# Performance work log

Hardware: AMD Instinct MI355X
Metric: run time of the kernel (lower is better)

The kernel has to match this reference:

```python
import jax, jax.numpy as jnp
import numpy as np

MARGIN_POS = 0.1
MARGIN_NEG = 0.8
HARD_RATIO = 0.3


def setup_inputs() -> dict:
    key = jax.random.key(0)
    k1, k2, k3 = jax.random.split(key, 3)
    B, D = 16384, 1024
    return {
        "q_neg_proj": jax.random.normal(k1, (B, D), dtype=jnp.float32),
        "d_pos": jax.random.normal(k2, (B, D), dtype=jnp.float32),
        "d_neg": jax.random.normal(k3, (B, D), dtype=jnp.float32),
    }


def reference(q_neg_proj, d_pos, d_neg):
    B = q_neg_proj.shape[0]
    num_hard = max(1, int(B * HARD_RATIO))

    # diag(q @ d.T) == rowwise dot product; avoid the BxB matmul
    diag_sim_pos = jnp.einsum("bd,bd->b", q_neg_proj, d_pos)
    diag_sim_neg = jnp.einsum("bd,bd->b", q_neg_proj, d_neg)

    # hardest positives: largest similarities
    hard_sim_pos, _ = jax.lax.top_k(diag_sim_pos, num_hard)
    loss_pos = jnp.mean(jax.nn.relu(hard_sim_pos - MARGIN_POS))

    # hardest negatives: smallest similarities (topk largest=False)
    neg_smallest, _ = jax.lax.top_k(-diag_sim_neg, num_hard)
    hard_sim_neg = -neg_smallest
    loss_neg = jnp.mean(jax.nn.relu(MARGIN_NEG - hard_sim_neg))

    total_loss = loss_pos + loss_neg
    return (total_loss, loss_pos, loss_neg)
```

## Files before the change

kernel.cpp:

```cpp
#include <hip/hip_runtime.h>

constexpr int B_ROWS = 16384;
constexpr int K_HARD = 4915;
constexpr float MARGIN_POS = 0.1f;
constexpr float MARGIN_NEG = 0.8f;

__global__ __launch_bounds__(256, 8) void dot_kernel(
    const float4* __restrict__ q,
    const float4* __restrict__ dp,
    const float4* __restrict__ dn,
    float* __restrict__ out_pos,
    float* __restrict__ out_neg)
{
    const int wave = (blockIdx.x * blockDim.x + threadIdx.x) >> 6;
    const int lane = threadIdx.x & 63;
    const int base = wave * 256 + lane;

    float4 qv[4], pv[4], nv[4];
#pragma unroll
    for (int it = 0; it < 4; ++it) qv[it] = q[base + it * 64];
#pragma unroll
    for (int it = 0; it < 4; ++it) pv[it] = dp[base + it * 64];
#pragma unroll
    for (int it = 0; it < 4; ++it) nv[it] = dn[base + it * 64];

    float sp = 0.f, sn = 0.f;
#pragma unroll
    for (int it = 0; it < 4; ++it) {
        sp += qv[it].x * pv[it].x + qv[it].y * pv[it].y
            + qv[it].z * pv[it].z + qv[it].w * pv[it].w;
        sn += qv[it].x * nv[it].x + qv[it].y * nv[it].y
            + qv[it].z * nv[it].z + qv[it].w * nv[it].w;
    }
#pragma unroll
    for (int off = 32; off; off >>= 1) {
        sp += __shfl_xor(sp, off);
        sn += __shfl_xor(sn, off);
    }
    if (lane == 0) {
        out_pos[wave] = sp;
        out_neg[wave] = sn;
    }
}

__device__ __forceinline__ unsigned f2key(float f) {
    unsigned u = __float_as_uint(f);
    return (u & 0x80000000u) ? ~u : (u | 0x80000000u);
}
__device__ __forceinline__ float key2f(unsigned k) {
    return __uint_as_float((k & 0x80000000u) ? (k & 0x7FFFFFFFu) : ~k);
}

__global__ __launch_bounds__(1024) void select_finalize_kernel(
    const float* __restrict__ ws_vals,
    float* __restrict__ out)
{
    __shared__ unsigned hist[256];
    __shared__ unsigned ebase[256];
    __shared__ unsigned s_prefix, s_m;
    __shared__ float    s_redf[16];
    __shared__ int      s_redc[16];
    __shared__ float    s_loss[2];

    const int tid  = threadIdx.x;
    const int lane = tid & 63;
    const int wid  = tid >> 6;

    for (int side = 0; side < 2; ++side) {
        const float4* v4 = (const float4*)(ws_vals + side * B_ROWS);

        unsigned key[16];
#pragma unroll
        for (int j = 0; j < 4; ++j) {
            float4 x = v4[tid + j * 1024];
            key[4 * j + 0] = f2key(x.x);
            key[4 * j + 1] = f2key(x.y);
            key[4 * j + 2] = f2key(x.z);
            key[4 * j + 3] = f2key(x.w);
        }

        unsigned m = side ? (unsigned)(K_HARD - 1) : (unsigned)(B_ROWS - K_HARD);
        unsigned prefix = 0;

        for (int r = 0; r < 4; ++r) {
            const unsigned shift = 24 - 8 * r;
            const unsigned pmask = (r == 0) ? 0u : (0xFFFFFFFFu << (32 - 8 * r));
            if (tid < 256) hist[tid] = 0;
            __syncthreads();
#pragma unroll
            for (int j = 0; j < 16; ++j)
                if ((key[j] & pmask) == prefix)
                    atomicAdd(&hist[(key[j] >> shift) & 255u], 1u);
            __syncthreads();

            if (wid == 0) {
                unsigned h0 = hist[4 * lane + 0];
                unsigned h1 = hist[4 * lane + 1];
                unsigned h2 = hist[4 * lane + 2];
                unsigned h3 = hist[4 * lane + 3];
                unsigned gsum = h0 + h1 + h2 + h3;
                unsigned inc = gsum;
#pragma unroll
                for (int off = 1; off < 64; off <<= 1) {
                    unsigned t = __shfl_up(inc, off);
                    if (lane >= off) inc += t;
                }
                unsigned ex = inc - gsum;
                ebase[4 * lane + 0] = ex;
                ebase[4 * lane + 1] = ex + h0;
                ebase[4 * lane + 2] = ex + h0 + h1;
                ebase[4 * lane + 3] = ex + h0 + h1 + h2;
            }
            __syncthreads();

            if (tid < 256) {
                unsigned lo = ebase[tid];
                unsigned hi = lo + hist[tid];
                if (lo <= m && m < hi) {
                    s_prefix = prefix | ((unsigned)tid << shift);
                    s_m = m - lo;
                }
            }
            __syncthreads();
            prefix = s_prefix;
            m = s_m;
        }

        const unsigned tkey = prefix;
        const float    tval = key2f(tkey);

        float lsum = 0.f;
        int cnt = 0;
#pragma unroll
        for (int j = 0; j < 16; ++j) {
            const bool sel = side ? (key[j] < tkey) : (key[j] > tkey);
            if (sel) {
                const float v = key2f(key[j]);
                lsum += side ? fmaxf(MARGIN_NEG - v, 0.f)
                             : fmaxf(v - MARGIN_POS, 0.f);
                cnt++;
            }
        }
#pragma unroll
        for (int off = 32; off; off >>= 1) {
            lsum += __shfl_xor(lsum, off);
            cnt  += __shfl_xor(cnt, off);
        }
        if (lane == 0) { s_redf[wid] = lsum; s_redc[wid] = cnt; }
        __syncthreads();
        if (tid == 0) {
            float tot = 0.f;
            int c = 0;
            for (int w = 0; w < 16; ++w) { tot += s_redf[w]; c += s_redc[w]; }
            const float ft = side ? fmaxf(MARGIN_NEG - tval, 0.f)
                                  : fmaxf(tval - MARGIN_POS, 0.f);
            s_loss[side] = (tot + (float)(K_HARD - c) * ft) / (float)K_HARD;
        }
        __syncthreads();
    }

    if (tid == 0) {
        const float lp = s_loss[0];
        const float ln = s_loss[1];
        out[0] = lp + ln;
        out[1] = lp;
        out[2] = ln;
    }
}

extern "C" void kernel_launch(void* const* d_in, const int* in_sizes, int n_in,
                              void* d_out, int out_size, void* d_ws, size_t ws_size,
                              hipStream_t stream) {
    const float4* q  = (const float4*)d_in[0];
    const float4* dp = (const float4*)d_in[1];
    const float4* dn = (const float4*)d_in[2];
    float* out = (float*)d_out;

    float* ws     = (float*)d_ws;
    float* ws_pos = ws;
    float* ws_neg = ws + B_ROWS;

    dot_kernel<<<(B_ROWS * 64) / 256, 256, 0, stream>>>(q, dp, dn, ws_pos, ws_neg);
    select_finalize_kernel<<<1, 1024, 0, stream>>>(ws_pos, out);
}
```

Before: 55.51 us.

## Issue dot loads via inline asm and run both radix selects together

The dot-product kernel now issues all twelve 16-byte global loads back-to-back in inline assembly with immediate offsets and a single wait, so every load is in flight at once. The selection kernel now runs the positive and negative radix-select passes interleaved in one loop over shared histograms, which halves the number of barrier-separated rounds in the single-block finalize. The inline asm bypasses compiler scheduling and assumes 32-bit offsets fit the buffers.

```diff
diff --git a/kernel.cpp b/kernel.cpp
--- a/kernel.cpp
+++ b/kernel.cpp
@@ -5,32 +5,52 @@
 constexpr float MARGIN_POS = 0.1f;
 constexpr float MARGIN_NEG = 0.8f;
 
+typedef float f32x4 __attribute__((ext_vector_type(4)));
+
 __global__ __launch_bounds__(256, 8) void dot_kernel(
-    const float4* __restrict__ q,
-    const float4* __restrict__ dp,
-    const float4* __restrict__ dn,
+    const float* __restrict__ q,
+    const float* __restrict__ dp,
+    const float* __restrict__ dn,
     float* __restrict__ out_pos,
     float* __restrict__ out_neg)
 {
     const int wave = (blockIdx.x * blockDim.x + threadIdx.x) >> 6;
     const int lane = threadIdx.x & 63;
-    const int base = wave * 256 + lane;
-
-    float4 qv[4], pv[4], nv[4];
-#pragma unroll
-    for (int it = 0; it < 4; ++it) qv[it] = q[base + it * 64];
-#pragma unroll
-    for (int it = 0; it < 4; ++it) pv[it] = dp[base + it * 64];
-#pragma unroll
-    for (int it = 0; it < 4; ++it) nv[it] = dn[base + it * 64];
+    const unsigned voff = (unsigned)wave * 4096u + (unsigned)lane * 16u;
+
+    f32x4 q0, q1, q2, q3, p0, p1, p2, p3, n0, n1, n2, n3;
+    asm volatile(
+        "global_load_dwordx4 %[Q0], %[VO], %[QB] offset:0\n\t"
+        "global_load_dwordx4 %[Q1], %[VO], %[QB] offset:1024\n\t"
+        "global_load_dwordx4 %[Q2], %[VO], %[QB] offset:2048\n\t"
+        "global_load_dwordx4 %[Q3], %[VO], %[QB] offset:3072\n\t"
+        "global_load_dwordx4 %[P0], %[VO], %[PB] offset:0\n\t"
+        "global_load_dwordx4 %[P1], %[VO], %[PB] offset:1024\n\t"
+        "global_load_dwordx4 %[P2], %[VO], %[PB] offset:2048\n\t"
+        "global_load_dwordx4 %[P3], %[VO], %[PB] offset:3072\n\t"
+        "global_load_dwordx4 %[N0], %[VO], %[NB] offset:0\n\t"
+        "global_load_dwordx4 %[N1], %[VO], %[NB] offset:1024\n\t"
+        "global_load_dwordx4 %[N2], %[VO], %[NB] offset:2048\n\t"
+        "global_load_dwordx4 %[N3], %[VO], %[NB] offset:3072\n\t"
+        "s_waitcnt vmcnt(0)"
+        : [Q0]"=&v"(q0), [Q1]"=&v"(q1), [Q2]"=&v"(q2), [Q3]"=&v"(q3),
+          [P0]"=&v"(p0), [P1]"=&v"(p1), [P2]"=&v"(p2), [P3]"=&v"(p3),
+          [N0]"=&v"(n0), [N1]"=&v"(n1), [N2]"=&v"(n2), [N3]"=&v"(n3)
+        : [VO]"v"(voff), [QB]"s"(q), [PB]"s"(dp), [NB]"s"(dn)
+    );
+
+    f32x4 qa[4] = {q0, q1, q2, q3};
+    f32x4 pa[4] = {p0, p1, p2, p3};
+    f32x4 na[4] = {n0, n1, n2, n3};
 
     float sp = 0.f, sn = 0.f;
 #pragma unroll
     for (int it = 0; it < 4; ++it) {
-        sp += qv[it].x * pv[it].x + qv[it].y * pv[it].y
-            + qv[it].z * pv[it].z + qv[it].w * pv[it].w;
-        sn += qv[it].x * nv[it].x + qv[it].y * nv[it].y
-            + qv[it].z * nv[it].z + qv[it].w * nv[it].w;
+#pragma unroll
+        for (int c = 0; c < 4; ++c) {
+            sp += qa[it][c] * pa[it][c];
+            sn += qa[it][c] * na[it][c];
+        }
     }
 #pragma unroll
     for (int off = 32; off; off >>= 1) {
@@ -55,125 +75,123 @@
     const float* __restrict__ ws_vals,
     float* __restrict__ out)
 {
-    __shared__ unsigned hist[256];
-    __shared__ unsigned ebase[256];
-    __shared__ unsigned s_prefix, s_m;
-    __shared__ float    s_redf[16];
-    __shared__ int      s_redc[16];
-    __shared__ float    s_loss[2];
+    __shared__ unsigned hist[2][256];
+    __shared__ unsigned ebase[2][256];
+    __shared__ unsigned s_prefix[2], s_m[2];
+    __shared__ float    s_rf[2][16];
+    __shared__ unsigned s_rc[2][16];
 
     const int tid  = threadIdx.x;
     const int lane = tid & 63;
     const int wid  = tid >> 6;
 
-    for (int side = 0; side < 2; ++side) {
-        const float4* v4 = (const float4*)(ws_vals + side * B_ROWS);
-
-        unsigned key[16];
-#pragma unroll
-        for (int j = 0; j < 4; ++j) {
-            float4 x = v4[tid + j * 1024];
-            key[4 * j + 0] = f2key(x.x);
-            key[4 * j + 1] = f2key(x.y);
-            key[4 * j + 2] = f2key(x.z);
-            key[4 * j + 3] = f2key(x.w);
-        }
-
-        unsigned m = side ? (unsigned)(K_HARD - 1) : (unsigned)(B_ROWS - K_HARD);
-        unsigned prefix = 0;
-
-        for (int r = 0; r < 4; ++r) {
-            const unsigned shift = 24 - 8 * r;
-            const unsigned pmask = (r == 0) ? 0u : (0xFFFFFFFFu << (32 - 8 * r));
-            if (tid < 256) hist[tid] = 0;
-            __syncthreads();
-#pragma unroll
-            for (int j = 0; j < 16; ++j)
-                if ((key[j] & pmask) == prefix)
-                    atomicAdd(&hist[(key[j] >> shift) & 255u], 1u);
-            __syncthreads();
-
-            if (wid == 0) {
-                unsigned h0 = hist[4 * lane + 0];
-                unsigned h1 = hist[4 * lane + 1];
-                unsigned h2 = hist[4 * lane + 2];
-                unsigned h3 = hist[4 * lane + 3];
-                unsigned gsum = h0 + h1 + h2 + h3;
-                unsigned inc = gsum;
-#pragma unroll
-                for (int off = 1; off < 64; off <<= 1) {
-                    unsigned t = __shfl_up(inc, off);
-                    if (lane >= off) inc += t;
-                }
-                unsigned ex = inc - gsum;
-                ebase[4 * lane + 0] = ex;
-                ebase[4 * lane + 1] = ex + h0;
-                ebase[4 * lane + 2] = ex + h0 + h1;
-                ebase[4 * lane + 3] = ex + h0 + h1 + h2;
+    const float4* vp = (const float4*)ws_vals;
+    const float4* vn = (const float4*)(ws_vals + B_ROWS);
+
+    unsigned kp[16], kn[16];
+#pragma unroll
+    for (int j = 0; j < 4; ++j) {
+        const float4 a = vp[tid + j * 1024];
+        const float4 b = vn[tid + j * 1024];
+        kp[4*j+0] = f2key(a.x); kp[4*j+1] = f2key(a.y);
+        kp[4*j+2] = f2key(a.z); kp[4*j+3] = f2key(a.w);
+        kn[4*j+0] = f2key(b.x); kn[4*j+1] = f2key(b.y);
+        kn[4*j+2] = f2key(b.z); kn[4*j+3] = f2key(b.w);
+    }
+
+    unsigned m0 = (unsigned)(B_ROWS - K_HARD), pre0 = 0;
+    unsigned m1 = (unsigned)(K_HARD - 1),      pre1 = 0;
+
+    for (int r = 0; r < 4; ++r) {
+        const unsigned shift = 24 - 8 * r;
+        const unsigned pmask = (r == 0) ? 0u : (0xFFFFFFFFu << (32 - 8 * r));
+        if (tid < 256) { hist[0][tid] = 0; hist[1][tid] = 0; }
+        __syncthreads();
+#pragma unroll
+        for (int j = 0; j < 16; ++j) {
+            if ((kp[j] & pmask) == pre0) atomicAdd(&hist[0][(kp[j] >> shift) & 255u], 1u);
+            if ((kn[j] & pmask) == pre1) atomicAdd(&hist[1][(kn[j] >> shift) & 255u], 1u);
+        }
+        __syncthreads();
+
+        if (wid < 2) {
+            const int s = wid;
+            const unsigned h0 = hist[s][4*lane+0], h1 = hist[s][4*lane+1];
+            const unsigned h2 = hist[s][4*lane+2], h3 = hist[s][4*lane+3];
+            const unsigned g = h0 + h1 + h2 + h3;
+            unsigned inc = g;
+#pragma unroll
+            for (int off = 1; off < 64; off <<= 1) {
+                const unsigned t = __shfl_up(inc, off);
+                if (lane >= off) inc += t;
             }
-            __syncthreads();
-
-            if (tid < 256) {
-                unsigned lo = ebase[tid];
-                unsigned hi = lo + hist[tid];
-                if (lo <= m && m < hi) {
-                    s_prefix = prefix | ((unsigned)tid << shift);
-                    s_m = m - lo;
-                }
+            const unsigned ex = inc - g;
+            ebase[s][4*lane+0] = ex;
+            ebase[s][4*lane+1] = ex + h0;
+            ebase[s][4*lane+2] = ex + h0 + h1;
+            ebase[s][4*lane+3] = ex + h0 + h1 + h2;
+        }
+        __syncthreads();
+
+        if (tid < 512) {
+            const int s = tid >> 8;
+            const int b = tid & 255;
+            const unsigned mm = s ? m1 : m0;
+            const unsigned lo = ebase[s][b];
+            const unsigned hi = lo + hist[s][b];
+            if (lo <= mm && mm < hi) {
+                s_prefix[s] = (s ? pre1 : pre0) | ((unsigned)b << shift);
+                s_m[s] = mm - lo;
             }
-            __syncthreads();
-            prefix = s_prefix;
-            m = s_m;
-        }
-
-        const unsigned tkey = prefix;
-        const float    tval = key2f(tkey);
-
-        float lsum = 0.f;
-        int cnt = 0;
-#pragma unroll
-        for (int j = 0; j < 16; ++j) {
-            const bool sel = side ? (key[j] < tkey) : (key[j] > tkey);
-            if (sel) {
-                const float v = key2f(key[j]);
-                lsum += side ? fmaxf(MARGIN_NEG - v, 0.f)
-                             : fmaxf(v - MARGIN_POS, 0.f);
-                cnt++;
-            }
-        }
-#pragma unroll
-        for (int off = 32; off; off >>= 1) {
-            lsum += __shfl_xor(lsum, off);
-            cnt  += __shfl_xor(cnt, off);
-        }
-        if (lane == 0) { s_redf[wid] = lsum; s_redc[wid] = cnt; }
-        __syncthreads();
-        if (tid == 0) {
-            float tot = 0.f;
-            int c = 0;
-            for (int w = 0; w < 16; ++w) { tot += s_redf[w]; c += s_redc[w]; }
-            const float ft = side ? fmaxf(MARGIN_NEG - tval, 0.f)
-                                  : fmaxf(tval - MARGIN_POS, 0.f);
-            s_loss[side] = (tot + (float)(K_HARD - c) * ft) / (float)K_HARD;
-        }
-        __syncthreads();
-    }
-
+        }
+        __syncthreads();
+        pre0 = s_prefix[0]; m0 = s_m[0];
+        pre1 = s_prefix[1]; m1 = s_m[1];
+    }
+
+    const unsigned tk0 = pre0, tk1 = pre1;
+    const float    tv0 = key2f(tk0), tv1 = key2f(tk1);
+
+    float lp = 0.f, ln = 0.f;
+    unsigned cp = 0, cn = 0;
+#pragma unroll
+    for (int j = 0; j < 16; ++j) {
+        if (kp[j] > tk0) { lp += fmaxf(key2f(kp[j]) - MARGIN_POS, 0.f); cp++; }
+        if (kn[j] < tk1) { ln += fmaxf(MARGIN_NEG - key2f(kn[j]), 0.f); cn++; }
+    }
+#pragma unroll
+    for (int off = 32; off; off >>= 1) {
+        lp += __shfl_xor(lp, off);  ln += __shfl_xor(ln, off);
+        cp += __shfl_xor(cp, off);  cn += __shfl_xor(cn, off);
+    }
+    if (lane == 0) {
+        s_rf[0][wid] = lp; s_rf[1][wid] = ln;
+        s_rc[0][wid] = cp; s_rc[1][wid] = cn;
+    }
+    __syncthreads();
     if (tid == 0) {
-        const float lp = s_loss[0];
-        const float ln = s_loss[1];
-        out[0] = lp + ln;
-        out[1] = lp;
-        out[2] = ln;
+        float tp = 0.f, tn = 0.f;
+        unsigned ccp = 0, ccn = 0;
+        for (int w = 0; w < 16; ++w) {
+            tp += s_rf[0][w]; tn += s_rf[1][w];
+            ccp += s_rc[0][w]; ccn += s_rc[1][w];
+        }
+        const float fp = fmaxf(tv0 - MARGIN_POS, 0.f);
+        const float fn = fmaxf(MARGIN_NEG - tv1, 0.f);
+        const float LP = (tp + (float)(K_HARD - (int)ccp) * fp) / (float)K_HARD;
+        const float LN = (tn + (float)(K_HARD - (int)ccn) * fn) / (float)K_HARD;
+        out[0] = LP + LN;
+        out[1] = LP;
+        out[2] = LN;
     }
 }
 
 extern "C" void kernel_launch(void* const* d_in, const int* in_sizes, int n_in,
                               void* d_out, int out_size, void* d_ws, size_t ws_size,
                               hipStream_t stream) {
-    const float4* q  = (const float4*)d_in[0];
-    const float4* dp = (const float4*)d_in[1];
-    const float4* dn = (const float4*)d_in[2];
+    const float* q  = (const float*)d_in[0];
+    const float* dp = (const float*)d_in[1];
+    const float* dn = (const float*)d_in[2];
     float* out = (float*)d_out;
 
     float* ws     = (float*)d_ws;
```

Result: faster. 52.79 us (-4.9%).

## Split selection across two blocks and hand-issue vector loads with inline asm

Applied to the files above, without the earlier changes.

The selection kernel now runs each side (positive and negative) in its own block instead of looping serially in one block. Completion uses an atomic ticket: the last block to finish combines the two losses, and the dot kernel resets the ticket. The dot kernel also issues its twelve dwordx4 loads through inline assembly with immediate offsets, marking the negative loads non-temporal, to keep all loads in flight. The aim is to halve the serial single-block selection latency, at the cost of relying on ticket ordering across kernels and a hard vmcnt(0) wait inside the asm.

```diff
diff --git a/kernel.cpp b/kernel.cpp
--- a/kernel.cpp
+++ b/kernel.cpp
@@ -5,32 +5,58 @@
 constexpr float MARGIN_POS = 0.1f;
 constexpr float MARGIN_NEG = 0.8f;
 
+typedef float f32x4 __attribute__((ext_vector_type(4)));
+
 __global__ __launch_bounds__(256, 8) void dot_kernel(
-    const float4* __restrict__ q,
-    const float4* __restrict__ dp,
-    const float4* __restrict__ dn,
+    const float* __restrict__ q,
+    const float* __restrict__ dp,
+    const float* __restrict__ dn,
     float* __restrict__ out_pos,
-    float* __restrict__ out_neg)
+    float* __restrict__ out_neg,
+    int* __restrict__ ticket)
 {
     const int wave = (blockIdx.x * blockDim.x + threadIdx.x) >> 6;
     const int lane = threadIdx.x & 63;
-    const int base = wave * 256 + lane;
-
-    float4 qv[4], pv[4], nv[4];
-#pragma unroll
-    for (int it = 0; it < 4; ++it) qv[it] = q[base + it * 64];
-#pragma unroll
-    for (int it = 0; it < 4; ++it) pv[it] = dp[base + it * 64];
-#pragma unroll
-    for (int it = 0; it < 4; ++it) nv[it] = dn[base + it * 64];
+
+    if (blockIdx.x == 0 && threadIdx.x == 0) {
+        __hip_atomic_store(ticket, 0, __ATOMIC_RELAXED, __HIP_MEMORY_SCOPE_AGENT);
+    }
+
+    const unsigned voff = (unsigned)wave * 4096u + (unsigned)lane * 16u;
+
+    f32x4 q0, q1, q2, q3, p0, p1, p2, p3, n0, n1, n2, n3;
+    asm volatile(
+        "global_load_dwordx4 %[Q0], %[VO], %[QB] offset:0\n\t"
+        "global_load_dwordx4 %[Q1], %[VO], %[QB] offset:1024\n\t"
+        "global_load_dwordx4 %[Q2], %[VO], %[QB] offset:2048\n\t"
+        "global_load_dwordx4 %[Q3], %[VO], %[QB] offset:3072\n\t"
+        "global_load_dwordx4 %[P0], %[VO], %[PB] offset:0\n\t"
+        "global_load_dwordx4 %[P1], %[VO], %[PB] offset:1024\n\t"
+        "global_load_dwordx4 %[P2], %[VO], %[PB] offset:2048\n\t"
+        "global_load_dwordx4 %[P3], %[VO], %[PB] offset:3072\n\t"
+        "global_load_dwordx4 %[N0], %[VO], %[NB] offset:0 nt\n\t"
+        "global_load_dwordx4 %[N1], %[VO], %[NB] offset:1024 nt\n\t"
+        "global_load_dwordx4 %[N2], %[VO], %[NB] offset:2048 nt\n\t"
+        "global_load_dwordx4 %[N3], %[VO], %[NB] offset:3072 nt\n\t"
+        "s_waitcnt vmcnt(0)"
+        : [Q0]"=&v"(q0), [Q1]"=&v"(q1), [Q2]"=&v"(q2), [Q3]"=&v"(q3),
+          [P0]"=&v"(p0), [P1]"=&v"(p1), [P2]"=&v"(p2), [P3]"=&v"(p3),
+          [N0]"=&v"(n0), [N1]"=&v"(n1), [N2]"=&v"(n2), [N3]"=&v"(n3)
+        : [VO]"v"(voff), [QB]"s"(q), [PB]"s"(dp), [NB]"s"(dn)
+    );
+
+    f32x4 qa[4] = {q0, q1, q2, q3};
+    f32x4 pa[4] = {p0, p1, p2, p3};
+    f32x4 na[4] = {n0, n1, n2, n3};
 
     float sp = 0.f, sn = 0.f;
 #pragma unroll
     for (int it = 0; it < 4; ++it) {
-        sp += qv[it].x * pv[it].x + qv[it].y * pv[it].y
-            + qv[it].z * pv[it].z + qv[it].w * pv[it].w;
-        sn += qv[it].x * nv[it].x + qv[it].y * nv[it].y
-            + qv[it].z * nv[it].z + qv[it].w * nv[it].w;
+#pragma unroll
+        for (int c = 0; c < 4; ++c) {
+            sp += qa[it][c] * pa[it][c];
+            sn += qa[it][c] * na[it][c];
+        }
     }
 #pragma unroll
     for (int off = 32; off; off >>= 1) {
@@ -51,135 +77,136 @@
     return __uint_as_float((k & 0x80000000u) ? (k & 0x7FFFFFFFu) : ~k);
 }
 
-__global__ __launch_bounds__(1024) void select_finalize_kernel(
+__global__ __launch_bounds__(1024) void select_kernel(
     const float* __restrict__ ws_vals,
-    float* __restrict__ out)
+    float* __restrict__ out,
+    int* __restrict__ ticket)
 {
     __shared__ unsigned hist[256];
     __shared__ unsigned ebase[256];
     __shared__ unsigned s_prefix, s_m;
-    __shared__ float    s_redf[16];
-    __shared__ int      s_redc[16];
-    __shared__ float    s_loss[2];
-
+    __shared__ float    s_rf[16];
+    __shared__ unsigned s_rc[16];
+
+    const int side = blockIdx.x;
     const int tid  = threadIdx.x;
     const int lane = tid & 63;
     const int wid  = tid >> 6;
 
-    for (int side = 0; side < 2; ++side) {
-        const float4* v4 = (const float4*)(ws_vals + side * B_ROWS);
-
-        unsigned key[16];
-#pragma unroll
-        for (int j = 0; j < 4; ++j) {
-            float4 x = v4[tid + j * 1024];
-            key[4 * j + 0] = f2key(x.x);
-            key[4 * j + 1] = f2key(x.y);
-            key[4 * j + 2] = f2key(x.z);
-            key[4 * j + 3] = f2key(x.w);
-        }
-
-        unsigned m = side ? (unsigned)(K_HARD - 1) : (unsigned)(B_ROWS - K_HARD);
-        unsigned prefix = 0;
-
-        for (int r = 0; r < 4; ++r) {
-            const unsigned shift = 24 - 8 * r;
-            const unsigned pmask = (r == 0) ? 0u : (0xFFFFFFFFu << (32 - 8 * r));
-            if (tid < 256) hist[tid] = 0;
-            __syncthreads();
-#pragma unroll
-            for (int j = 0; j < 16; ++j)
-                if ((key[j] & pmask) == prefix)
-                    atomicAdd(&hist[(key[j] >> shift) & 255u], 1u);
-            __syncthreads();
-
-            if (wid == 0) {
-                unsigned h0 = hist[4 * lane + 0];
-                unsigned h1 = hist[4 * lane + 1];
-                unsigned h2 = hist[4 * lane + 2];
-                unsigned h3 = hist[4 * lane + 3];
-                unsigned gsum = h0 + h1 + h2 + h3;
-                unsigned inc = gsum;
-#pragma unroll
-                for (int off = 1; off < 64; off <<= 1) {
-                    unsigned t = __shfl_up(inc, off);
-                    if (lane >= off) inc += t;
-                }
-                unsigned ex = inc - gsum;
-                ebase[4 * lane + 0] = ex;
-                ebase[4 * lane + 1] = ex + h0;
-                ebase[4 * lane + 2] = ex + h0 + h1;
-                ebase[4 * lane + 3] = ex + h0 + h1 + h2;
+    const float4* v4 = (const float4*)(ws_vals + side * B_ROWS);
+
+    unsigned key[16];
+#pragma unroll
+    for (int j = 0; j < 4; ++j) {
+        const float4 a = v4[tid + j * 1024];
+        key[4*j+0] = f2key(a.x); key[4*j+1] = f2key(a.y);
+        key[4*j+2] = f2key(a.z); key[4*j+3] = f2key(a.w);
+    }
+
+    unsigned m = side ? (unsigned)(K_HARD - 1) : (unsigned)(B_ROWS - K_HARD);
+    unsigned prefix = 0;
+
+    for (int r = 0; r < 4; ++r) {
+        const unsigned shift = 24 - 8 * r;
+        const unsigned pmask = (r == 0) ? 0u : (0xFFFFFFFFu << (32 - 8 * r));
+        if (tid < 256) hist[tid] = 0;
+        __syncthreads();
+#pragma unroll
+        for (int j = 0; j < 16; ++j)
+            if ((key[j] & pmask) == prefix)
+                atomicAdd(&hist[(key[j] >> shift) & 255u], 1u);
+        __syncthreads();
+
+        if (wid == 0) {
+            const unsigned h0 = hist[4*lane+0], h1 = hist[4*lane+1];
+            const unsigned h2 = hist[4*lane+2], h3 = hist[4*lane+3];
+            const unsigned g = h0 + h1 + h2 + h3;
+            unsigned inc = g;
+#pragma unroll
+            for (int off = 1; off < 64; off <<= 1) {
+                const unsigned t = __shfl_up(inc, off);
+                if (lane >= off) inc += t;
             }
-            __syncthreads();
-
-            if (tid < 256) {
-                unsigned lo = ebase[tid];
-                unsigned hi = lo + hist[tid];
-                if (lo <= m && m < hi) {
-                    s_prefix = prefix | ((unsigned)tid << shift);
-                    s_m = m - lo;
-                }
+            const unsigned ex = inc - g;
+            ebase[4*lane+0] = ex;
+            ebase[4*lane+1] = ex + h0;
+            ebase[4*lane+2] = ex + h0 + h1;
+            ebase[4*lane+3] = ex + h0 + h1 + h2;
+        }
+        __syncthreads();
+
+        if (tid < 256) {
+            const unsigned lo = ebase[tid];
+            const unsigned hi = lo + hist[tid];
+            if (lo <= m && m < hi) {
+                s_prefix = prefix | ((unsigned)tid << shift);
+                s_m = m - lo;
             }
-            __syncthreads();
-            prefix = s_prefix;
-            m = s_m;
-        }
-
-        const unsigned tkey = prefix;
-        const float    tval = key2f(tkey);
-
-        float lsum = 0.f;
-        int cnt = 0;
-#pragma unroll
-        for (int j = 0; j < 16; ++j) {
-            const bool sel = side ? (key[j] < tkey) : (key[j] > tkey);
-            if (sel) {
-                const float v = key2f(key[j]);
-                lsum += side ? fmaxf(MARGIN_NEG - v, 0.f)
-                             : fmaxf(v - MARGIN_POS, 0.f);
-                cnt++;
-            }
-        }
-#pragma unroll
-        for (int off = 32; off; off >>= 1) {
-            lsum += __shfl_xor(lsum, off);
-            cnt  += __shfl_xor(cnt, off);
-        }
-        if (lane == 0) { s_redf[wid] = lsum; s_redc[wid] = cnt; }
-        __syncthreads();
-        if (tid == 0) {
-            float tot = 0.f;
-            int c = 0;
-            for (int w = 0; w < 16; ++w) { tot += s_redf[w]; c += s_redc[w]; }
-            const float ft = side ? fmaxf(MARGIN_NEG - tval, 0.f)
-                                  : fmaxf(tval - MARGIN_POS, 0.f);
-            s_loss[side] = (tot + (float)(K_HARD - c) * ft) / (float)K_HARD;
-        }
-        __syncthreads();
-    }
+        }
+        __syncthreads();
+        prefix = s_prefix;
+        m = s_m;
+    }
+
+    const unsigned tkey = prefix;
+    const float    tval = key2f(tkey);
+
+    float lsum = 0.f;
+    unsigned cnt = 0;
+#pragma unroll
+    for (int j = 0; j < 16; ++j) {
+        const bool sel = side ? (key[j] < tkey) : (key[j] > tkey);
+        if (sel) {
+            const float v = key2f(key[j]);
+            lsum += side ? fmaxf(MARGIN_NEG - v, 0.f)
+                         : fmaxf(v - MARGIN_POS, 0.f);
+            cnt++;
+        }
+    }
+#pragma unroll
+    for (int off = 32; off; off >>= 1) {
+        lsum += __shfl_xor(lsum, off);
+        cnt  += __shfl_xor(cnt, off);
+    }
+    if (lane == 0) { s_rf[wid] = lsum; s_rc[wid] = cnt; }
+    __syncthreads();
 
     if (tid == 0) {
-        const float lp = s_loss[0];
-        const float ln = s_loss[1];
-        out[0] = lp + ln;
-        out[1] = lp;
-        out[2] = ln;
+        float tot = 0.f;
+        unsigned c = 0;
+        for (int w = 0; w < 16; ++w) { tot += s_rf[w]; c += s_rc[w]; }
+        const float ft = side ? fmaxf(MARGIN_NEG - tval, 0.f)
+                              : fmaxf(tval - MARGIN_POS, 0.f);
+        const float loss = (tot + (float)(K_HARD - (int)c) * ft) / (float)K_HARD;
+
+        __hip_atomic_store(&out[1 + side], loss,
+                           __ATOMIC_RELEASE, __HIP_MEMORY_SCOPE_AGENT);
+        const int t = __hip_atomic_fetch_add(ticket, 1,
+                           __ATOMIC_ACQ_REL, __HIP_MEMORY_SCOPE_AGENT);
+        if (t == 1) {
+            const float lp = __hip_atomic_load(&out[1],
+                                __ATOMIC_ACQUIRE, __HIP_MEMORY_SCOPE_AGENT);
+            const float ln = __hip_atomic_load(&out[2],
+                                __ATOMIC_ACQUIRE, __HIP_MEMORY_SCOPE_AGENT);
+            __hip_atomic_store(&out[0], lp + ln,
+                               __ATOMIC_RELAXED, __HIP_MEMORY_SCOPE_AGENT);
+        }
     }
 }
 
 extern "C" void kernel_launch(void* const* d_in, const int* in_sizes, int n_in,
                               void* d_out, int out_size, void* d_ws, size_t ws_size,
                               hipStream_t stream) {
-    const float4* q  = (const float4*)d_in[0];
-    const float4* dp = (const float4*)d_in[1];
-    const float4* dn = (const float4*)d_in[2];
+    const float* q  = (const float*)d_in[0];
+    const float* dp = (const float*)d_in[1];
+    const float* dn = (const float*)d_in[2];
     float* out = (float*)d_out;
 
     float* ws     = (float*)d_ws;
     float* ws_pos = ws;
     float* ws_neg = ws + B_ROWS;
-
-    dot_kernel<<<(B_ROWS * 64) / 256, 256, 0, stream>>>(q, dp, dn, ws_pos, ws_neg);
-    select_finalize_kernel<<<1, 1024, 0, stream>>>(ws_pos, out);
-}
+    int*   ticket = (int*)(ws + 2 * B_ROWS);
+
+    dot_kernel<<<(B_ROWS * 64) / 256, 256, 0, stream>>>(q, dp, dn, ws_pos, ws_neg, ticket);
+    select_kernel<<<2, 1024, 0, stream>>>(ws_pos, out, ticket);
+}
```

Result: faster. 47.35 us (-14.7%).
